# Optimization experiments

Measured on AMD Instinct MI355X. Metric: run time of the kernel, lower is better.

Reference implementation:

```python
import jax, jax.numpy as jnp
import numpy as np

N_NODES = 50000
DIM = 128
N_EDGES = 800000
N_UID = 4096
ORDER = 3
LN_EPS = 1e-5


def setup_inputs() -> dict:
    key = jax.random.key(0)
    ks = jax.random.split(key, 6)
    scale = 1.0 / np.sqrt(DIM)
    embedding = jax.random.normal(ks[0], (N_NODES, DIM), jnp.float32) * np.sqrt(2.0 / DIM)  # kaiming-ish
    W = jax.random.normal(ks[1], (ORDER, DIM, DIM), jnp.float32) * scale
    b = jnp.zeros((ORDER, DIM), jnp.float32)
    gamma = jnp.ones((ORDER, DIM), jnp.float32)
    beta = jnp.zeros((ORDER, DIM), jnp.float32)
    src = jax.random.randint(ks[2], (N_EDGES,), 0, N_NODES, jnp.int32)
    dst = jax.random.randint(ks[3], (N_EDGES,), 0, N_NODES, jnp.int32)
    uid = jax.random.randint(ks[4], (N_UID,), 0, N_NODES, jnp.int32)
    return {"embedding": embedding, "W": W, "b": b, "gamma": gamma,
            "beta": beta, "src": src, "dst": dst, "uid": uid}


def _layer_norm(x, g, bta):
    mu = jnp.mean(x, axis=-1, keepdims=True)
    var = jnp.var(x, axis=-1, keepdims=True)
    return (x - mu) * jax.lax.rsqrt(var + LN_EPS) * g + bta


def reference(embedding, W, b, gamma, beta, src, dst, uid):
    # in-degree per destination node (DGL 'gcn' aggregator uses in_degrees)
    deg = jax.ops.segment_sum(jnp.ones((src.shape[0],), embedding.dtype), dst,
                              num_segments=N_NODES)  # [N]
    inv = (1.0 / (deg + 1.0))[:, None]  # [N,1]
    feats = embedding
    for i in range(ORDER):
        # gather source features, scatter-sum into destinations
        neigh = jax.ops.segment_sum(feats[src], dst, num_segments=N_NODES)  # [N,D]
        h = (neigh + feats) * inv                    # gcn-style mean incl. self
        h = jnp.einsum('nd,ed->ne', h, W[i]) + b[i]  # fc_neigh
        feats = jax.nn.elu(_layer_norm(h, gamma[i], beta[i]))
    return feats[uid]  # [N_UID, D]
```

## Files before the change

kernel.cpp:

```cpp
#include <hip/hip_runtime.h>
#include <math.h>

typedef unsigned int   uint;
typedef unsigned short ushort;

#define N_NODES 50000
#define DIM     128
#define N_EDGES 800000
#define N_UID   4096
#define LN_EPS  1e-5f
#define RST     132
#define XST     136
#define NBUCK   196
#define PCHUNK  4096

typedef __attribute__((ext_vector_type(8))) short bf16x8;
typedef __attribute__((ext_vector_type(4))) float f32x4;
typedef __attribute__((ext_vector_type(4))) uint  u32x4;

__device__ __forceinline__ float bf_lo(uint u) { return __builtin_bit_cast(float, u << 16); }
__device__ __forceinline__ float bf_hi(uint u) { return __builtin_bit_cast(float, u & 0xffff0000u); }
__device__ __forceinline__ uint pack_bf16(float a, float b) {
    uint ua = __builtin_bit_cast(uint, a);
    uint ub = __builtin_bit_cast(uint, b);
    uint ra = (ua + 0x7fffu + ((ua >> 16) & 1u)) >> 16;
    uint rb = (ub + 0x7fffu + ((ub >> 16) & 1u)) >> 16;
    return ra | (rb << 16);
}

__global__ __launch_bounds__(256) void prep_kernel(const float* __restrict__ emb, ushort* __restrict__ E,
                                                   const float* __restrict__ W, ushort* __restrict__ WB,
                                                   int* __restrict__ bhist) {
    int i = blockIdx.x * 256 + threadIdx.x;
    if (i < N_NODES * DIM / 4) {
        const float4 v = ((const float4*)emb)[i];
        uint2 p;
        p.x = pack_bf16(v.x, v.y);
        p.y = pack_bf16(v.z, v.w);
        ((uint2*)E)[i] = p;
    }
    if (i < 3 * DIM * DIM / 4) {
        const float4 v = ((const float4*)W)[i];
        uint2 p;
        p.x = pack_bf16(v.x, v.y);
        p.y = pack_bf16(v.z, v.w);
        ((uint2*)WB)[i] = p;
    }
    if (i < NBUCK) bhist[i] = 0;
}

__global__ __launch_bounds__(256) void bhist_kernel(const int* __restrict__ dst, int* __restrict__ bhist) {
    __shared__ int h[256];
    const int t = threadIdx.x;
    h[t] = 0;
    __syncthreads();
    for (int e = blockIdx.x * 256 + t; e < N_EDGES; e += gridDim.x * 256)
        atomicAdd(&h[dst[e] >> 8], 1);
    __syncthreads();
    if (t < NBUCK && h[t]) atomicAdd(&bhist[t], h[t]);
}

__global__ __launch_bounds__(256) void bscan_kernel(const int* __restrict__ bhist, int* __restrict__ bbase,
                                                    int* __restrict__ bcur, int* __restrict__ off) {
    __shared__ int sh[256];
    const int t = threadIdx.x;
    const int v = (t < NBUCK) ? bhist[t] : 0;
    sh[t] = v;
    __syncthreads();
    for (int o = 1; o < 256; o <<= 1) {
        int x = (t >= o) ? sh[t - o] : 0;
        __syncthreads();
        sh[t] += x;
        __syncthreads();
    }
    const int excl = sh[t] - v;
    if (t < NBUCK) { bbase[t] = excl; bcur[t] = excl; }
    if (t == NBUCK - 1) bbase[NBUCK] = excl + v;
    if (t == 0) off[N_NODES] = N_EDGES;
}

__global__ __launch_bounds__(256) void part_kernel(const int* __restrict__ src, const int* __restrict__ dst,
                                                   int* __restrict__ bcur, int2* __restrict__ pak) {
    __shared__ int h[256];
    __shared__ int base[256];
    __shared__ int cur[256];
    const int t  = threadIdx.x;
    const int e0 = blockIdx.x * PCHUNK;
    const int e1 = min(e0 + PCHUNK, N_EDGES);
    h[t] = 0;
    __syncthreads();
    for (int i = e0 + t; i < e1; i += 256)
        atomicAdd(&h[dst[i] >> 8], 1);
    __syncthreads();
    if (t < NBUCK && h[t]) base[t] = atomicAdd(&bcur[t], h[t]);
    cur[t] = 0;
    __syncthreads();
    for (int i = e0 + t; i < e1; i += 256) {
        const int s = src[i], d = dst[i];
        const int b = d >> 8;
        const int q = atomicAdd(&cur[b], 1);
        pak[base[b] + q] = make_int2(s, d);
    }
}

__global__ __launch_bounds__(256) void bucket_kernel(const int2* __restrict__ pak, const int* __restrict__ bbase,
                                                     int* __restrict__ off, int* __restrict__ csr) {
    __shared__ int cnt[256];
    __shared__ int pos[256];
    const int b = blockIdx.x, t = threadIdx.x;
    const int e0 = bbase[b], e1 = bbase[b + 1], m = e1 - e0;
    cnt[t] = 0;
    __syncthreads();
    for (int i = t; i < m; i += 256) atomicAdd(&cnt[pak[e0 + i].y & 255], 1);
    __syncthreads();
    const int v = cnt[t];
    pos[t] = v;
    __syncthreads();
    for (int o = 1; o < 256; o <<= 1) {
        int x = (t >= o) ? pos[t - o] : 0;
        __syncthreads();
        pos[t] += x;
        __syncthreads();
    }
    const int excl = pos[t] - v;
    const int node = b * 256 + t;
    if (node < N_NODES) off[node] = e0 + excl;
    __syncthreads();
    pos[t] = excl;
    __syncthreads();
    for (int i = t; i < m; i += 256) {
        const int2 p = pak[e0 + i];
        const int q = atomicAdd(&pos[p.y & 255], 1);
        csr[e0 + q] = p.x;
    }
}

template <bool OUT_BF16>
__global__ __launch_bounds__(512) void layer_kernel(
    const ushort* __restrict__ fin, void* __restrict__ fout,
    const int* __restrict__ off, const int* __restrict__ csr,
    const int* __restrict__ uidmap, const ushort* __restrict__ wb,
    const float* __restrict__ bias, const float* __restrict__ gamma,
    const float* __restrict__ beta, int nrows)
{
    __shared__ ushort xs[32 * XST];
    __shared__ float  ys[32 * RST];
    const int t = threadIdx.x;
    const int rows = blockIdx.x * 32;

    {
        const int lx   = t & 15;
        const int st   = t >> 4;
        const int slot = rows + st;
        const bool valid = slot < nrows;
        const int n  = valid ? (uidmap ? uidmap[slot] : slot) : 0;
        const int d0 = off[n];
        int d1 = off[n + 1];
        if (!valid) d1 = d0;
        const int deg = d1 - d0;

        float a[8];
        {
            const uint4 q = ((const uint4*)(fin + (size_t)n * DIM))[lx];
            a[0]=bf_lo(q.x); a[1]=bf_hi(q.x); a[2]=bf_lo(q.y); a[3]=bf_hi(q.y);
            a[4]=bf_lo(q.z); a[5]=bf_hi(q.z); a[6]=bf_lo(q.w); a[7]=bf_hi(q.w);
        }

        const int nfull = deg >> 3;
        int e = d0;
        int id[8];
        if (nfull > 0) {
            #pragma unroll
            for (int k = 0; k < 8; ++k) id[k] = csr[e + k];
        }
        for (int r = 0; r < nfull; ++r) {
            uint4 v[8];
            #pragma unroll
            for (int k = 0; k < 8; ++k)
                v[k] = ((const uint4*)(fin + (size_t)id[k] * DIM))[lx];
            int idn[8];
            if (r + 1 < nfull) {
                #pragma unroll
                for (int k = 0; k < 8; ++k) idn[k] = csr[e + 8 + k];
            }
            #pragma unroll
            for (int k = 0; k < 8; ++k) {
                a[0] += bf_lo(v[k].x); a[1] += bf_hi(v[k].x);
                a[2] += bf_lo(v[k].y); a[3] += bf_hi(v[k].y);
                a[4] += bf_lo(v[k].z); a[5] += bf_hi(v[k].z);
                a[6] += bf_lo(v[k].w); a[7] += bf_hi(v[k].w);
            }
            if (r + 1 < nfull) {
                #pragma unroll
                for (int k = 0; k < 8; ++k) id[k] = idn[k];
            }
            e += 8;
        }
        if (e < d1) {
            const int last = d1 - 1;
            int   idt[8];
            float m[8];
            #pragma unroll
            for (int k = 0; k < 8; ++k) {
                const int ee = e + k;
                idt[k] = csr[(ee <= last) ? ee : last];
                m[k]   = (ee <= last) ? 1.0f : 0.0f;
            }
            uint4 v[8];
            #pragma unroll
            for (int k = 0; k < 8; ++k)
                v[k] = ((const uint4*)(fin + (size_t)idt[k] * DIM))[lx];
            #pragma unroll
            for (int k = 0; k < 8; ++k) {
                a[0] = fmaf(m[k], bf_lo(v[k].x), a[0]); a[1] = fmaf(m[k], bf_hi(v[k].x), a[1]);
                a[2] = fmaf(m[k], bf_lo(v[k].y), a[2]); a[3] = fmaf(m[k], bf_hi(v[k].y), a[3]);
                a[4] = fmaf(m[k], bf_lo(v[k].z), a[4]); a[5] = fmaf(m[k], bf_hi(v[k].z), a[5]);
                a[6] = fmaf(m[k], bf_lo(v[k].w), a[6]); a[7] = fmaf(m[k], bf_hi(v[k].w), a[7]);
            }
        }

        const float iv = 1.0f / (float)(deg + 1);
        uint4 p;
        p.x = pack_bf16(a[0] * iv, a[1] * iv);
        p.y = pack_bf16(a[2] * iv, a[3] * iv);
        p.z = pack_bf16(a[4] * iv, a[5] * iv);
        p.w = pack_bf16(a[6] * iv, a[7] * iv);
        *((uint4*)(xs + st * XST + lx * 8)) = p;
    }
    __syncthreads();

    {
        const int wave = t >> 6, lane = t & 63;
        const int row_off = (wave >> 2) * 16;
        const int col_off = (wave & 3) * 32;
        const int lm   = lane & 15;
        const int quad = lane >> 4;
        f32x4 acc[2] = {f32x4{0,0,0,0}, f32x4{0,0,0,0}};
        const ushort* xrow = xs + (row_off + lm) * XST + quad * 8;
        const ushort* __restrict__ wrow = wb + (size_t)(col_off + lm) * DIM + quad * 8;
        #pragma unroll
        for (int kk = 0; kk < 4; ++kk) {
            const bf16x8 af = __builtin_bit_cast(bf16x8, *(const u32x4*)(xrow + kk * 32));
            #pragma unroll
            for (int c = 0; c < 2; ++c) {
                const bf16x8 bf = __builtin_bit_cast(bf16x8,
                    *(const u32x4*)(wrow + (size_t)c * 16 * DIM + kk * 32));
                acc[c] = __builtin_amdgcn_mfma_f32_16x16x32_bf16(af, bf, acc[c], 0, 0, 0);
            }
        }
        #pragma unroll
        for (int c = 0; c < 2; ++c) {
            #pragma unroll
            for (int r = 0; r < 4; ++r)
                ys[(row_off + quad * 4 + r) * RST + col_off + c * 16 + lm] = acc[c][r];
        }
    }
    __syncthreads();

    {
        const int r   = t >> 4;
        const int seg = t & 15;
        const int db  = seg * 8;
        const float* yr = ys + r * RST + db;
        float vs[8];
        {
            const float4 y0 = ((const float4*)yr)[0];
            const float4 y1 = ((const float4*)yr)[1];
            const float4 b0 = ((const float4*)(bias + db))[0];
            const float4 b1 = ((const float4*)(bias + db))[1];
            vs[0] = y0.x + b0.x; vs[1] = y0.y + b0.y; vs[2] = y0.z + b0.z; vs[3] = y0.w + b0.w;
            vs[4] = y1.x + b1.x; vs[5] = y1.y + b1.y; vs[6] = y1.z + b1.z; vs[7] = y1.w + b1.w;
        }
        float s1 = 0.0f, s2 = 0.0f;
        #pragma unroll
        for (int i = 0; i < 8; ++i) { s1 += vs[i]; s2 += vs[i] * vs[i]; }
        #pragma unroll
        for (int m = 1; m < 16; m <<= 1) {
            s1 += __shfl_xor(s1, m);
            s2 += __shfl_xor(s2, m);
        }
        const float mu  = s1 * (1.0f / 128.0f);
        const float var = s2 * (1.0f / 128.0f) - mu * mu;
        const float rs  = rsqrtf(var + LN_EPS);
        float ov[8];
        {
            const float4 g0 = ((const float4*)(gamma + db))[0];
            const float4 g1 = ((const float4*)(gamma + db))[1];
            const float4 t0 = ((const float4*)(beta + db))[0];
            const float4 t1 = ((const float4*)(beta + db))[1];
            float z;
            z = (vs[0] - mu) * rs * g0.x + t0.x; ov[0] = (z > 0.0f) ? z : expm1f(z);
            z = (vs[1] - mu) * rs * g0.y + t0.y; ov[1] = (z > 0.0f) ? z : expm1f(z);
            z = (vs[2] - mu) * rs * g0.z + t0.z; ov[2] = (z > 0.0f) ? z : expm1f(z);
            z = (vs[3] - mu) * rs * g0.w + t0.w; ov[3] = (z > 0.0f) ? z : expm1f(z);
            z = (vs[4] - mu) * rs * g1.x + t1.x; ov[4] = (z > 0.0f) ? z : expm1f(z);
            z = (vs[5] - mu) * rs * g1.y + t1.y; ov[5] = (z > 0.0f) ? z : expm1f(z);
            z = (vs[6] - mu) * rs * g1.z + t1.z; ov[6] = (z > 0.0f) ? z : expm1f(z);
            z = (vs[7] - mu) * rs * g1.w + t1.w; ov[7] = (z > 0.0f) ? z : expm1f(z);
        }
        const int n = rows + r;
        if (n < nrows) {
            if (OUT_BF16) {
                uint4 p;
                p.x = pack_bf16(ov[0], ov[1]);
                p.y = pack_bf16(ov[2], ov[3]);
                p.z = pack_bf16(ov[4], ov[5]);
                p.w = pack_bf16(ov[6], ov[7]);
                *((uint4*)((ushort*)fout + (size_t)n * DIM + db)) = p;
            } else {
                float* op = (float*)fout + (size_t)n * DIM + db;
                ((float4*)op)[0] = make_float4(ov[0], ov[1], ov[2], ov[3]);
                ((float4*)op)[1] = make_float4(ov[4], ov[5], ov[6], ov[7]);
            }
        }
    }
}

extern "C" void kernel_launch(void* const* d_in, const int* in_sizes, int n_in,
                              void* d_out, int out_size, void* d_ws, size_t ws_size,
                              hipStream_t stream) {
    const float* emb   = (const float*)d_in[0];
    const float* W     = (const float*)d_in[1];
    const float* bias  = (const float*)d_in[2];
    const float* gamma = (const float*)d_in[3];
    const float* beta  = (const float*)d_in[4];
    const int*   src   = (const int*)d_in[5];
    const int*   dst   = (const int*)d_in[6];
    const int*   uid   = (const int*)d_in[7];

    ushort* E    = (ushort*)d_ws;
    ushort* A    = E + (size_t)N_NODES * DIM;
    ushort* B    = A + (size_t)N_NODES * DIM;
    ushort* WB   = B + (size_t)N_NODES * DIM;
    int*    off  = (int*)(WB + 3 * DIM * DIM);
    int*    bhist = off + (N_NODES + 4);
    int*    bbase = bhist + 256;
    int*    bcur  = bbase + 260;
    int2*   pak   = (int2*)(bcur + 256);
    int*    csr   = (int*)(pak + N_EDGES);

    prep_kernel<<<(N_NODES * DIM / 4 + 255) / 256, 256, 0, stream>>>(emb, E, W, WB, bhist);
    bhist_kernel<<<512, 256, 0, stream>>>(dst, bhist);
    bscan_kernel<<<1, 256, 0, stream>>>(bhist, bbase, bcur, off);
    part_kernel<<<(N_EDGES + PCHUNK - 1) / PCHUNK, 256, 0, stream>>>(src, dst, bcur, pak);
    bucket_kernel<<<NBUCK, 256, 0, stream>>>(pak, bbase, off, csr);

    const int lblk = (N_NODES + 31) / 32;
    layer_kernel<true><<<lblk, 512, 0, stream>>>(E, A, off, csr, nullptr, WB,
                                                 bias, gamma, beta, N_NODES);
    layer_kernel<true><<<lblk, 512, 0, stream>>>(A, B, off, csr, nullptr, WB + DIM * DIM,
                                                 bias + DIM, gamma + DIM, beta + DIM, N_NODES);
    layer_kernel<false><<<N_UID / 32, 512, 0, stream>>>(B, (float*)d_out, off, csr, uid,
                                                        WB + 2 * DIM * DIM, bias + 2 * DIM,
                                                        gamma + 2 * DIM, beta + 2 * DIM, N_UID);
}
```

Measured before the change: 230.1 us.

## Split fused layer into separate aggregation and GEMM+LayerNorm kernels

Each layer's fused gather-then-MFMA kernel is split into an aggregation kernel (256 threads, 16 rows per block) that writes mean-aggregated bf16 rows to global memory, and a GEMM+LayerNorm kernel that reads its A operand directly from global memory and writes the result in place. The tail-edge path is replaced by padding with a zeroed sentinel row at index N_NODES, so no masking multiply is needed. ELU now uses __expf(z)-1 instead of expm1f. The split is meant to give the latency-bound gather better occupancy, at the cost of an extra global round trip and three extra launches per forward.

Result: slower. 245.1 us (+6.5%).

```diff
diff --git a/kernel.cpp b/kernel.cpp
--- a/kernel.cpp
+++ b/kernel.cpp
@@ -10,12 +10,12 @@
 #define N_UID   4096
 #define LN_EPS  1e-5f
 #define RST     132
-#define XST     136
 #define NBUCK   196
 #define PCHUNK  4096
 
 typedef __attribute__((ext_vector_type(8))) short bf16x8;
 typedef __attribute__((ext_vector_type(4))) float f32x4;
+typedef __attribute__((ext_vector_type(2))) float f32x2;
 typedef __attribute__((ext_vector_type(4))) uint  u32x4;
 
 __device__ __forceinline__ float bf_lo(uint u) { return __builtin_bit_cast(float, u << 16); }
@@ -30,7 +30,8 @@
 
 __global__ __launch_bounds__(256) void prep_kernel(const float* __restrict__ emb, ushort* __restrict__ E,
                                                    const float* __restrict__ W, ushort* __restrict__ WB,
-                                                   int* __restrict__ bhist) {
+                                                   int* __restrict__ bhist,
+                                                   ushort* __restrict__ T1, ushort* __restrict__ T2) {
     int i = blockIdx.x * 256 + threadIdx.x;
     if (i < N_NODES * DIM / 4) {
         const float4 v = ((const float4*)emb)[i];
@@ -47,6 +48,12 @@
         ((uint2*)WB)[i] = p;
     }
     if (i < NBUCK) bhist[i] = 0;
+    if (i < DIM / 4) {
+        const uint2 z = make_uint2(0u, 0u);
+        ((uint2*)(E  + (size_t)N_NODES * DIM))[i] = z;
+        ((uint2*)(T1 + (size_t)N_NODES * DIM))[i] = z;
+        ((uint2*)(T2 + (size_t)N_NODES * DIM))[i] = z;
+    }
 }
 
 __global__ __launch_bounds__(256) void bhist_kernel(const int* __restrict__ dst, int* __restrict__ bhist) {
@@ -135,99 +142,81 @@
     }
 }
 
+__global__ __launch_bounds__(256) void agg_kernel(
+    const ushort* __restrict__ fin, ushort* __restrict__ xm,
+    const int* __restrict__ off, const int* __restrict__ csr,
+    const int* __restrict__ uidmap, int nrows)
+{
+    const int t    = threadIdx.x;
+    const int lx   = t & 15;
+    const int st   = t >> 4;
+    const int slot = blockIdx.x * 16 + st;
+    if (slot >= nrows) return;
+    const int n = uidmap ? uidmap[slot] : slot;
+
+    const uint4 q0 = ((const uint4*)(fin + (size_t)n * DIM))[lx];
+    const int d0 = off[n];
+    const int d1 = off[n + 1];
+    const int deg = d1 - d0;
+
+    f32x2 a[4];
+    a[0] = f32x2{bf_lo(q0.x), bf_hi(q0.x)};
+    a[1] = f32x2{bf_lo(q0.y), bf_hi(q0.y)};
+    a[2] = f32x2{bf_lo(q0.z), bf_hi(q0.z)};
+    a[3] = f32x2{bf_lo(q0.w), bf_hi(q0.w)};
+
+    const int rounds = (deg + 7) >> 3;
+    int id[8];
+    int e = d0;
+    if (rounds > 0) {
+        #pragma unroll
+        for (int k = 0; k < 8; ++k) {
+            const int ee = e + k;
+            const int c = csr[ee];
+            id[k] = (ee < d1) ? c : N_NODES;
+        }
+    }
+    for (int r = 0; r < rounds; ++r) {
+        uint4 v[8];
+        #pragma unroll
+        for (int k = 0; k < 8; ++k)
+            v[k] = ((const uint4*)(fin + (size_t)id[k] * DIM))[lx];
+        if (r + 1 < rounds) {
+            #pragma unroll
+            for (int k = 0; k < 8; ++k) {
+                const int ee = e + 8 + k;
+                const int c = csr[ee];
+                id[k] = (ee < d1) ? c : N_NODES;
+            }
+        }
+        #pragma unroll
+        for (int k = 0; k < 8; ++k) {
+            a[0] += f32x2{bf_lo(v[k].x), bf_hi(v[k].x)};
+            a[1] += f32x2{bf_lo(v[k].y), bf_hi(v[k].y)};
+            a[2] += f32x2{bf_lo(v[k].z), bf_hi(v[k].z)};
+            a[3] += f32x2{bf_lo(v[k].w), bf_hi(v[k].w)};
+        }
+        e += 8;
+    }
+
+    const float iv = 1.0f / (float)(deg + 1);
+    uint4 p;
+    p.x = pack_bf16(a[0].x * iv, a[0].y * iv);
+    p.y = pack_bf16(a[1].x * iv, a[1].y * iv);
+    p.z = pack_bf16(a[2].x * iv, a[2].y * iv);
+    p.w = pack_bf16(a[3].x * iv, a[3].y * iv);
+    *((uint4*)(xm + (size_t)slot * DIM + lx * 8)) = p;
+}
+
 template <bool OUT_BF16>
-__global__ __launch_bounds__(512) void layer_kernel(
-    const ushort* __restrict__ fin, void* __restrict__ fout,
-    const int* __restrict__ off, const int* __restrict__ csr,
-    const int* __restrict__ uidmap, const ushort* __restrict__ wb,
-    const float* __restrict__ bias, const float* __restrict__ gamma,
-    const float* __restrict__ beta, int nrows)
+__global__ __launch_bounds__(512) void gemmln_kernel(
+    const ushort* xm, void* fout,
+    const ushort* __restrict__ wb, const float* __restrict__ bias,
+    const float* __restrict__ gamma, const float* __restrict__ beta, int nrows)
 {
-    __shared__ ushort xs[32 * XST];
-    __shared__ float  ys[32 * RST];
+    __shared__ float ys[32 * RST];
     const int t = threadIdx.x;
     const int rows = blockIdx.x * 32;
-
-    {
-        const int lx   = t & 15;
-        const int st   = t >> 4;
-        const int slot = rows + st;
-        const bool valid = slot < nrows;
-        const int n  = valid ? (uidmap ? uidmap[slot] : slot) : 0;
-        const int d0 = off[n];
-        int d1 = off[n + 1];
-        if (!valid) d1 = d0;
-        const int deg = d1 - d0;
-
-        float a[8];
-        {
-            const uint4 q = ((const uint4*)(fin + (size_t)n * DIM))[lx];
-            a[0]=bf_lo(q.x); a[1]=bf_hi(q.x); a[2]=bf_lo(q.y); a[3]=bf_hi(q.y);
-            a[4]=bf_lo(q.z); a[5]=bf_hi(q.z); a[6]=bf_lo(q.w); a[7]=bf_hi(q.w);
-        }
-
-        const int nfull = deg >> 3;
-        int e = d0;
-        int id[8];
-        if (nfull > 0) {
-            #pragma unroll
-            for (int k = 0; k < 8; ++k) id[k] = csr[e + k];
-        }
-        for (int r = 0; r < nfull; ++r) {
-            uint4 v[8];
-            #pragma unroll
-            for (int k = 0; k < 8; ++k)
-                v[k] = ((const uint4*)(fin + (size_t)id[k] * DIM))[lx];
-            int idn[8];
-            if (r + 1 < nfull) {
-                #pragma unroll
-                for (int k = 0; k < 8; ++k) idn[k] = csr[e + 8 + k];
-            }
-            #pragma unroll
-            for (int k = 0; k < 8; ++k) {
-                a[0] += bf_lo(v[k].x); a[1] += bf_hi(v[k].x);
-                a[2] += bf_lo(v[k].y); a[3] += bf_hi(v[k].y);
-                a[4] += bf_lo(v[k].z); a[5] += bf_hi(v[k].z);
-                a[6] += bf_lo(v[k].w); a[7] += bf_hi(v[k].w);
-            }
-            if (r + 1 < nfull) {
-                #pragma unroll
-                for (int k = 0; k < 8; ++k) id[k] = idn[k];
-            }
-            e += 8;
-        }
-        if (e < d1) {
-            const int last = d1 - 1;
-            int   idt[8];
-            float m[8];
-            #pragma unroll
-            for (int k = 0; k < 8; ++k) {
-                const int ee = e + k;
-                idt[k] = csr[(ee <= last) ? ee : last];
-                m[k]   = (ee <= last) ? 1.0f : 0.0f;
-            }
-            uint4 v[8];
-            #pragma unroll
-            for (int k = 0; k < 8; ++k)
-                v[k] = ((const uint4*)(fin + (size_t)idt[k] * DIM))[lx];
-            #pragma unroll
-            for (int k = 0; k < 8; ++k) {
-                a[0] = fmaf(m[k], bf_lo(v[k].x), a[0]); a[1] = fmaf(m[k], bf_hi(v[k].x), a[1]);
-                a[2] = fmaf(m[k], bf_lo(v[k].y), a[2]); a[3] = fmaf(m[k], bf_hi(v[k].y), a[3]);
-                a[4] = fmaf(m[k], bf_lo(v[k].z), a[4]); a[5] = fmaf(m[k], bf_hi(v[k].z), a[5]);
-                a[6] = fmaf(m[k], bf_lo(v[k].w), a[6]); a[7] = fmaf(m[k], bf_hi(v[k].w), a[7]);
-            }
-        }
-
-        const float iv = 1.0f / (float)(deg + 1);
-        uint4 p;
-        p.x = pack_bf16(a[0] * iv, a[1] * iv);
-        p.y = pack_bf16(a[2] * iv, a[3] * iv);
-        p.z = pack_bf16(a[4] * iv, a[5] * iv);
-        p.w = pack_bf16(a[6] * iv, a[7] * iv);
-        *((uint4*)(xs + st * XST + lx * 8)) = p;
-    }
-    __syncthreads();
 
     {
         const int wave = t >> 6, lane = t & 63;
@@ -235,17 +224,18 @@
         const int col_off = (wave & 3) * 32;
         const int lm   = lane & 15;
         const int quad = lane >> 4;
+        const int arow = min(rows + row_off + lm, nrows - 1);
+        const ushort* xrow = xm + (size_t)arow * DIM + quad * 8;
+        const ushort* wrow = wb + (size_t)(col_off + lm) * DIM + quad * 8;
         f32x4 acc[2] = {f32x4{0,0,0,0}, f32x4{0,0,0,0}};
-        const ushort* xrow = xs + (row_off + lm) * XST + quad * 8;
-        const ushort* __restrict__ wrow = wb + (size_t)(col_off + lm) * DIM + quad * 8;
         #pragma unroll
         for (int kk = 0; kk < 4; ++kk) {
             const bf16x8 af = __builtin_bit_cast(bf16x8, *(const u32x4*)(xrow + kk * 32));
             #pragma unroll
             for (int c = 0; c < 2; ++c) {
-                const bf16x8 bf = __builtin_bit_cast(bf16x8,
+                const bf16x8 bfr = __builtin_bit_cast(bf16x8,
                     *(const u32x4*)(wrow + (size_t)c * 16 * DIM + kk * 32));
-                acc[c] = __builtin_amdgcn_mfma_f32_16x16x32_bf16(af, bf, acc[c], 0, 0, 0);
+                acc[c] = __builtin_amdgcn_mfma_f32_16x16x32_bf16(af, bfr, acc[c], 0, 0, 0);
             }
         }
         #pragma unroll
@@ -289,14 +279,14 @@
             const float4 t0 = ((const float4*)(beta + db))[0];
             const float4 t1 = ((const float4*)(beta + db))[1];
             float z;
-            z = (vs[0] - mu) * rs * g0.x + t0.x; ov[0] = (z > 0.0f) ? z : expm1f(z);
-            z = (vs[1] - mu) * rs * g0.y + t0.y; ov[1] = (z > 0.0f) ? z : expm1f(z);
-            z = (vs[2] - mu) * rs * g0.z + t0.z; ov[2] = (z > 0.0f) ? z : expm1f(z);
-            z = (vs[3] - mu) * rs * g0.w + t0.w; ov[3] = (z > 0.0f) ? z : expm1f(z);
-            z = (vs[4] - mu) * rs * g1.x + t1.x; ov[4] = (z > 0.0f) ? z : expm1f(z);
-            z = (vs[5] - mu) * rs * g1.y + t1.y; ov[5] = (z > 0.0f) ? z : expm1f(z);
-            z = (vs[6] - mu) * rs * g1.z + t1.z; ov[6] = (z > 0.0f) ? z : expm1f(z);
-            z = (vs[7] - mu) * rs * g1.w + t1.w; ov[7] = (z > 0.0f) ? z : expm1f(z);
+            z = (vs[0] - mu) * rs * g0.x + t0.x; ov[0] = (z > 0.0f) ? z : __expf(z) - 1.0f;
+            z = (vs[1] - mu) * rs * g0.y + t0.y; ov[1] = (z > 0.0f) ? z : __expf(z) - 1.0f;
+            z = (vs[2] - mu) * rs * g0.z + t0.z; ov[2] = (z > 0.0f) ? z : __expf(z) - 1.0f;
+            z = (vs[3] - mu) * rs * g0.w + t0.w; ov[3] = (z > 0.0f) ? z : __expf(z) - 1.0f;
+            z = (vs[4] - mu) * rs * g1.x + t1.x; ov[4] = (z > 0.0f) ? z : __expf(z) - 1.0f;
+            z = (vs[5] - mu) * rs * g1.y + t1.y; ov[5] = (z > 0.0f) ? z : __expf(z) - 1.0f;
+            z = (vs[6] - mu) * rs * g1.z + t1.z; ov[6] = (z > 0.0f) ? z : __expf(z) - 1.0f;
+            z = (vs[7] - mu) * rs * g1.w + t1.w; ov[7] = (z > 0.0f) ? z : __expf(z) - 1.0f;
         }
         const int n = rows + r;
         if (n < nrows) {
@@ -328,10 +318,11 @@
     const int*   dst   = (const int*)d_in[6];
     const int*   uid   = (const int*)d_in[7];
 
+    const size_t FROW = (size_t)(N_NODES + 1) * DIM;
     ushort* E    = (ushort*)d_ws;
-    ushort* A    = E + (size_t)N_NODES * DIM;
-    ushort* B    = A + (size_t)N_NODES * DIM;
-    ushort* WB   = B + (size_t)N_NODES * DIM;
+    ushort* T1   = E + FROW;
+    ushort* T2   = T1 + FROW;
+    ushort* WB   = T2 + FROW;
     int*    off  = (int*)(WB + 3 * DIM * DIM);
     int*    bhist = off + (N_NODES + 4);
     int*    bbase = bhist + 256;
@@ -339,18 +330,22 @@
     int2*   pak   = (int2*)(bcur + 256);
     int*    csr   = (int*)(pak + N_EDGES);
 
-    prep_kernel<<<(N_NODES * DIM / 4 + 255) / 256, 256, 0, stream>>>(emb, E, W, WB, bhist);
+    prep_kernel<<<(N_NODES * DIM / 4 + 255) / 256, 256, 0, stream>>>(emb, E, W, WB, bhist, T1, T2);
     bhist_kernel<<<512, 256, 0, stream>>>(dst, bhist);
     bscan_kernel<<<1, 256, 0, stream>>>(bhist, bbase, bcur, off);
     part_kernel<<<(N_EDGES + PCHUNK - 1) / PCHUNK, 256, 0, stream>>>(src, dst, bcur, pak);
     bucket_kernel<<<NBUCK, 256, 0, stream>>>(pak, bbase, off, csr);
 
-    const int lblk = (N_NODES + 31) / 32;
-    layer_kernel<true><<<lblk, 512, 0, stream>>>(E, A, off, csr, nullptr, WB,
-                                                 bias, gamma, beta, N_NODES);
-    layer_kernel<true><<<lblk, 512, 0, stream>>>(A, B, off, csr, nullptr, WB + DIM * DIM,
-                                                 bias + DIM, gamma + DIM, beta + DIM, N_NODES);
-    layer_kernel<false><<<N_UID / 32, 512, 0, stream>>>(B, (float*)d_out, off, csr, uid,
-                                                        WB + 2 * DIM * DIM, bias + 2 * DIM,
-                                                        gamma + 2 * DIM, beta + 2 * DIM, N_UID);
-}
+    const int ablk = N_NODES / 16;
+    const int gblk = (N_NODES + 31) / 32;
+
+    agg_kernel<<<ablk, 256, 0, stream>>>(E, T1, off, csr, nullptr, N_NODES);
+    gemmln_kernel<true><<<gblk, 512, 0, stream>>>(T1, T1, WB, bias, gamma, beta, N_NODES);
+    agg_kernel<<<ablk, 256, 0, stream>>>(T1, T2, off, csr, nullptr, N_NODES);
+    gemmln_kernel<true><<<gblk, 512, 0, stream>>>(T2, T2, WB + DIM * DIM,
+                                                  bias + DIM, gamma + DIM, beta + DIM, N_NODES);
+    agg_kernel<<<N_UID / 16, 256, 0, stream>>>(T2, T1, off, csr, uid, N_UID);
+    gemmln_kernel<false><<<N_UID / 32, 512, 0, stream>>>(T1, (float*)d_out, WB + 2 * DIM * DIM,
+                                                         bias + 2 * DIM, gamma + 2 * DIM,
+                                                         beta + 2 * DIM, N_UID);
+}
```
